# Optimization experiments

Measured on AMD Instinct MI355X. Metric: run time of the kernel, lower is better.

## Reference

```python
import jax, jax.numpy as jnp
import numpy as np

N_NODES = 50000
N_EDGES = 640000
D_FEAT = 128
D_HID = 128


def _sage_conv(x, src, dst, W_l, b_l, W_r, num_nodes):
    """PyG SAGEConv (aggr='mean'): out = lin_l(mean_j x_j) + lin_r(x_i).

    W_l/W_r are [out, in] (torch Linear convention); lin_r has no bias.
    """
    msgs = x[src]                                               # [E, d]
    agg = jax.ops.segment_sum(msgs, dst, num_segments=num_nodes)
    cnt = jax.ops.segment_sum(jnp.ones((src.shape[0], 1), x.dtype), dst,
                              num_segments=num_nodes)           # [N, 1]
    mean = agg / jnp.maximum(cnt, 1.0)                          # [N, d]
    return mean @ W_l.T + b_l + x @ W_r.T


def setup_inputs() -> dict:
    key = jax.random.key(0)
    ks = jax.random.split(key, 8)
    x = jax.random.normal(ks[0], (N_NODES, D_FEAT), dtype=jnp.float32)
    edge_index = jax.random.randint(ks[1], (2, N_EDGES), 0, N_NODES, dtype=jnp.int64)
    s1 = 1.0 / np.sqrt(D_FEAT)
    s2 = 1.0 / np.sqrt(D_HID)
    W1_l = jax.random.uniform(ks[2], (D_HID, D_FEAT), jnp.float32, -s1, s1)
    b1_l = jnp.zeros((D_HID,), jnp.float32)
    W1_r = jax.random.uniform(ks[3], (D_HID, D_FEAT), jnp.float32, -s1, s1)
    W2_l = jax.random.uniform(ks[4], (D_HID, D_HID), jnp.float32, -s2, s2)
    b2_l = jnp.zeros((D_HID,), jnp.float32)
    W2_r = jax.random.uniform(ks[5], (D_HID, D_HID), jnp.float32, -s2, s2)
    return {"x": x, "edge_index": edge_index, "W1_l": W1_l, "b1_l": b1_l,
            "W1_r": W1_r, "W2_l": W2_l, "b2_l": b2_l, "W2_r": W2_r}


def reference(x, edge_index, W1_l, b1_l, W1_r, W2_l, b2_l, W2_r):
    src, dst = edge_index[0], edge_index[1]
    n = x.shape[0]
    h = _sage_conv(x, src, dst, W1_l, b1_l, W1_r, n)
    h = jax.nn.relu(h)
    h = _sage_conv(h, src, dst, W2_l, b2_l, W2_r, n)
    return jax.nn.relu(h)
```

## Files before the change

kernel.cpp:

```cpp
#include <hip/hip_runtime.h>
#include <hip/hip_bf16.h>

#define N_NODES 50000
#define N_EDGES 640000
#define D 128
#define SCAN_BLK 25
#define PSTRIDE 50048

typedef __bf16 bf16x8 __attribute__((ext_vector_type(8)));
typedef float f32x4 __attribute__((ext_vector_type(4)));

__device__ __forceinline__ ushort f2bf(float f) {
    __hip_bfloat16 h = __float2bfloat16(f);
    return *(ushort*)&h;
}
__device__ __forceinline__ float bflo(uint u) { return __uint_as_float(u << 16); }
__device__ __forceinline__ float bfhi(uint u) { return __uint_as_float(u & 0xffff0000u); }

__global__ __launch_bounds__(256) void zero_kernel(uint4* __restrict__ p) {
    p[blockIdx.x * 256 + threadIdx.x] = make_uint4(0u, 0u, 0u, 0u);
}

__global__ __launch_bounds__(256) void prep_kernel(const float* __restrict__ x,
                                                   const float* __restrict__ W1l,
                                                   const float* __restrict__ W1r,
                                                   const float* __restrict__ W2l,
                                                   const float* __restrict__ W2r,
                                                   const int* __restrict__ dst,
                                                   ushort* __restrict__ xb,
                                                   ushort* __restrict__ Wb1,
                                                   ushort* __restrict__ Wb2,
                                                   int* __restrict__ deg8,
                                                   int* __restrict__ rank) {
    const int b = blockIdx.x;
    const int tid = threadIdx.x;
    if (b < 625) {
        const int base = b * 1024 + tid;
        int* dp = deg8 + (b & 7) * PSTRIDE;
        int d0 = dst[base];
        int d1 = dst[base + 256];
        int d2 = dst[base + 512];
        int d3 = dst[base + 768];
        int r0 = atomicAdd(&dp[d0], 1);
        int r1 = atomicAdd(&dp[d1], 1);
        int r2 = atomicAdd(&dp[d2], 1);
        int r3 = atomicAdd(&dp[d3], 1);
        rank[base]       = r0;
        rank[base + 256] = r1;
        rank[base + 512] = r2;
        rank[base + 768] = r3;
    } else if (b < 3750) {
        int i = (b - 625) * 256 + tid;
        const float4 u0 = *(const float4*)&x[i * 8];
        const float4 u1 = *(const float4*)&x[i * 8 + 4];
        union { ushort u[8]; uint4 v; } p;
        p.u[0] = f2bf(u0.x); p.u[1] = f2bf(u0.y); p.u[2] = f2bf(u0.z); p.u[3] = f2bf(u0.w);
        p.u[4] = f2bf(u1.x); p.u[5] = f2bf(u1.y); p.u[6] = f2bf(u1.z); p.u[7] = f2bf(u1.w);
        *(uint4*)&xb[i * 8] = p.v;
    } else {
        int i = (b - 3750) * 256 + tid;
        if (i < 32768) {
            int n = i >> 8, k = i & 255;
            float v = (k < 128) ? W1l[n * 128 + k] : W1r[n * 128 + (k - 128)];
            Wb1[i] = f2bf(v);
        } else {
            int j = i - 32768;
            int n = j >> 8, k = j & 255;
            float v = (k < 128) ? W2l[n * 128 + k] : W2r[n * 128 + (k - 128)];
            Wb2[j] = f2bf(v);
        }
    }
}

__global__ __launch_bounds__(256) void scan1_kernel(const int* __restrict__ deg8,
                                                    int* __restrict__ incl,
                                                    int* __restrict__ blockSum) {
    __shared__ int wsum[4];
    const int t = threadIdx.x;
    const int base = blockIdx.x * 2048 + t * 8;
    int v[8];
    int s = 0;
#pragma unroll
    for (int i = 0; i < 8; ++i) {
        int idx = base + i;
        int tot = 0;
        if (idx < N_NODES) {
#pragma unroll
            for (int p = 0; p < 8; ++p) tot += deg8[p * PSTRIDE + idx];
        }
        v[i] = tot;
        s += tot;
    }
    const int lane = t & 63;
    const int wid = t >> 6;
    int ps = s;
#pragma unroll
    for (int off = 1; off < 64; off <<= 1) {
        int u = __shfl_up(ps, off, 64);
        if (lane >= off) ps += u;
    }
    if (lane == 63) wsum[wid] = ps;
    __syncthreads();
    int wOff = 0;
    for (int w = 0; w < wid; ++w) wOff += wsum[w];
    int run = wOff + ps - s;
#pragma unroll
    for (int i = 0; i < 8; ++i) {
        run += v[i];
        int idx = base + i;
        if (idx < N_NODES) incl[idx] = run;
    }
    if (t == 255) blockSum[blockIdx.x] = wOff + ps;
}

__global__ __launch_bounds__(256) void scan2_kernel(const int* __restrict__ deg8,
                                                    const int* __restrict__ incl,
                                                    const int* __restrict__ blockSum,
                                                    int* __restrict__ row_off,
                                                    int* __restrict__ cursor8) {
    const int b = blockIdx.x;
    int off = 0;
    for (int i = 0; i < b; ++i) off += blockSum[i];
    const int t = threadIdx.x;
#pragma unroll
    for (int i = 0; i < 8; ++i) {
        int idx = b * 2048 + i * 256 + t;
        if (idx < N_NODES) {
            int inc = incl[idx] + off;
            row_off[idx + 1] = inc;
            int dp[8];
            int dsum = 0;
#pragma unroll
            for (int p = 0; p < 8; ++p) { dp[p] = deg8[p * PSTRIDE + idx]; dsum += dp[p]; }
            int c = inc - dsum;
#pragma unroll
            for (int p = 0; p < 8; ++p) { cursor8[p * PSTRIDE + idx] = c; c += dp[p]; }
        }
    }
    if (b == 0 && t == 0) row_off[0] = 0;
}

__global__ __launch_bounds__(256) void fill_kernel(const int* __restrict__ src,
                                                   const int* __restrict__ dst,
                                                   const int* __restrict__ rank,
                                                   const int* __restrict__ cursor8,
                                                   int* __restrict__ esrc) {
    const int base = blockIdx.x * 1024 + threadIdx.x;
    const int* cp = cursor8 + (blockIdx.x & 7) * PSTRIDE;
    int d0 = dst[base];
    int d1 = dst[base + 256];
    int d2 = dst[base + 512];
    int d3 = dst[base + 768];
    int s0 = src[base];
    int s1 = src[base + 256];
    int s2 = src[base + 512];
    int s3 = src[base + 768];
    int r0 = rank[base];
    int r1 = rank[base + 256];
    int r2 = rank[base + 512];
    int r3 = rank[base + 768];
    esrc[cp[d0] + r0] = s0;
    esrc[cp[d1] + r1] = s1;
    esrc[cp[d2] + r2] = s2;
    esrc[cp[d3] + r3] = s3;
}

__global__ __launch_bounds__(256) void gather_mean(const int* __restrict__ row_off,
                                                   const int* __restrict__ esrc,
                                                   const ushort* __restrict__ feat,
                                                   ushort* __restrict__ mean) {
    const int node = (blockIdx.x * 256 + threadIdx.x) >> 6;
    const int lane = threadIdx.x & 63;
    if (node >= N_NODES) return;
    const int beg = row_off[node];
    const int end = row_off[node + 1];
    const int g = lane >> 4;
    const int c = lane & 15;
    const char* fb = (const char*)feat;
    float acc[8];
#pragma unroll
    for (int r = 0; r < 8; ++r) acc[r] = 0.0f;

    for (int base = beg; base < end; base += 64) {
        const int lim = min(end - base, 64);
        int myIdx = 0;
        if (lane < lim) myIdx = esrc[base + lane];
        for (int i0 = 0; i0 < lim; i0 += 16) {
            uint4 v[4];
#pragma unroll
            for (int u = 0; u < 4; ++u) {
                int slot = i0 + u * 4 + g;
                int s = __shfl(myIdx, slot, 64);
                v[u] = make_uint4(0u, 0u, 0u, 0u);
                if (slot < lim)
                    v[u] = *(const uint4*)(fb + ((size_t)s << 8) + c * 16);
            }
#pragma unroll
            for (int u = 0; u < 4; ++u) {
                acc[0] += bflo(v[u].x);
                acc[1] += bfhi(v[u].x);
                acc[2] += bflo(v[u].y);
                acc[3] += bfhi(v[u].y);
                acc[4] += bflo(v[u].z);
                acc[5] += bfhi(v[u].z);
                acc[6] += bflo(v[u].w);
                acc[7] += bfhi(v[u].w);
            }
        }
    }
#pragma unroll
    for (int r = 0; r < 8; ++r) {
        acc[r] += __shfl_xor(acc[r], 16, 64);
        acc[r] += __shfl_xor(acc[r], 32, 64);
    }
    if (g == 0) {
        const int dg = end - beg;
        const float inv = (dg > 0) ? 1.0f / (float)dg : 0.0f;
        union { ushort u[8]; uint4 v; } p;
#pragma unroll
        for (int r = 0; r < 8; ++r) p.u[r] = f2bf(acc[r] * inv);
        *(uint4*)((char*)mean + ((size_t)node << 8) + c * 16) = p.v;
    }
}

template <int OUT_BF16>
__global__ __launch_bounds__(256) void sage_mfma(const ushort* __restrict__ feat,
                                                 const ushort* __restrict__ mean,
                                                 const ushort* __restrict__ Wb,
                                                 const float* __restrict__ bias,
                                                 void* __restrict__ outv) {
    __shared__ __align__(16) char As[64 * 512];

    const int tid = threadIdx.x;
    const int nodeBase = blockIdx.x * 64;

    {
        const int row = tid >> 2;
        const int q = tid & 3;
        const int node = nodeBase + row;
        const bool valid = node < N_NODES;
        const ushort* srcp = (q < 2) ? (mean + (size_t)node * D + q * 64)
                                     : (feat + (size_t)node * D + (q - 2) * 64);
        const int swz = (row & 7) << 4;
#pragma unroll
        for (int c = 0; c < 8; ++c) {
            uint4 v = make_uint4(0u, 0u, 0u, 0u);
            if (valid) v = *(const uint4*)(srcp + c * 8);
            int colb = q * 128 + c * 16;
            *(uint4*)(As + row * 512 + (colb ^ swz)) = v;
        }
    }
    __syncthreads();

    const int lane = tid & 63;
    const int w = tid >> 6;
    const int l15 = lane & 15;
    const int lg = lane >> 4;
    const int swz = (l15 & 7) << 4;

    f32x4 acc[4][2];
#pragma unroll
    for (int m = 0; m < 4; ++m) {
        acc[m][0] = (f32x4)(0.0f);
        acc[m][1] = (f32x4)(0.0f);
    }

    const ushort* WA = Wb + (size_t)(w * 32 + l15) * 256 + lg * 8;
    const ushort* WB = WA + 16 * 256;

#pragma unroll
    for (int t = 0; t < 8; ++t) {
        bf16x8 b0 = *(const bf16x8*)(WA + t * 32);
        bf16x8 b1 = *(const bf16x8*)(WB + t * 32);
        const int kb = t * 64 + lg * 16;
#pragma unroll
        for (int m = 0; m < 4; ++m) {
            bf16x8 a = *(const bf16x8*)(As + (m * 16 + l15) * 512 + (kb ^ swz));
            acc[m][0] = __builtin_amdgcn_mfma_f32_16x16x32_bf16(a, b0, acc[m][0], 0, 0, 0);
            acc[m][1] = __builtin_amdgcn_mfma_f32_16x16x32_bf16(a, b1, acc[m][1], 0, 0, 0);
        }
    }

    const int c0 = w * 32 + l15;
    const float bv0 = bias[c0];
    const float bv1 = bias[c0 + 16];
#pragma unroll
    for (int m = 0; m < 4; ++m) {
#pragma unroll
        for (int j = 0; j < 4; ++j) {
            int node = nodeBase + m * 16 + lg * 4 + j;
            if (node < N_NODES) {
                float r0 = fmaxf(acc[m][0][j] + bv0, 0.0f);
                float r1 = fmaxf(acc[m][1][j] + bv1, 0.0f);
                if (OUT_BF16) {
                    ushort* out = (ushort*)outv;
                    out[(size_t)node * D + c0]      = f2bf(r0);
                    out[(size_t)node * D + c0 + 16] = f2bf(r1);
                } else {
                    float* out = (float*)outv;
                    out[(size_t)node * D + c0]      = r0;
                    out[(size_t)node * D + c0 + 16] = r1;
                }
            }
        }
    }
}

extern "C" void kernel_launch(void* const* d_in, const int* in_sizes, int n_in,
                              void* d_out, int out_size, void* d_ws, size_t ws_size,
                              hipStream_t stream) {
    const float* x   = (const float*)d_in[0];
    const int*   ei  = (const int*)d_in[1];
    const int*   src = ei;
    const int*   dst = ei + N_EDGES;
    const float* W1l = (const float*)d_in[2];
    const float* b1  = (const float*)d_in[3];
    const float* W1r = (const float*)d_in[4];
    const float* W2l = (const float*)d_in[5];
    const float* b2  = (const float*)d_in[6];
    const float* W2r = (const float*)d_in[7];
    float* out = (float*)d_out;

    ushort* xb     = (ushort*)d_ws;
    ushort* hb     = xb + (size_t)N_NODES * D;
    ushort* meanb  = hb + (size_t)N_NODES * D;
    int*   row_off = (int*)(meanb + (size_t)N_NODES * D);
    int*   esrc    = row_off + (N_NODES + 1);
    int*   rank    = esrc + N_EDGES;
    int*   deg8    = rank + N_EDGES;
    int*   cursor8 = deg8 + 8 * PSTRIDE;
    int*   incl    = cursor8 + 8 * PSTRIDE;
    int*   blockSum= incl + N_NODES;
    ushort* Wb1    = (ushort*)(blockSum + SCAN_BLK);
    ushort* Wb2    = Wb1 + 128 * 256;

    const int edge4Blocks = N_EDGES / 1024;
    const int waveBlocks = (N_NODES * 64 + 255) / 256;
    const int gemmBlocks = (N_NODES + 63) / 64;
    const int prepBlocks = 625 + 3125 + 256;
    const int zeroBlocks = (8 * PSTRIDE * 4) / 4096;

    zero_kernel<<<zeroBlocks, 256, 0, stream>>>((uint4*)deg8);
    prep_kernel<<<prepBlocks, 256, 0, stream>>>(x, W1l, W1r, W2l, W2r, dst,
                                                xb, Wb1, Wb2, deg8, rank);
    scan1_kernel<<<SCAN_BLK, 256, 0, stream>>>(deg8, incl, blockSum);
    scan2_kernel<<<SCAN_BLK, 256, 0, stream>>>(deg8, incl, blockSum, row_off, cursor8);
    fill_kernel<<<edge4Blocks, 256, 0, stream>>>(src, dst, rank, cursor8, esrc);

    gather_mean<<<waveBlocks, 256, 0, stream>>>(row_off, esrc, xb, meanb);
    sage_mfma<1><<<gemmBlocks, 256, 0, stream>>>(xb, meanb, Wb1, b1, hb);

    gather_mean<<<waveBlocks, 256, 0, stream>>>(row_off, esrc, hb, meanb);
    sage_mfma<0><<<gemmBlocks, 256, 0, stream>>>(hb, meanb, Wb2, b2, out);
}
```

Before: 149.4 us.

## Fuse CSR build kernels into one cooperative kernel with grid syncs

Replaces the five preprocessing launches (zero, prep, scan1, scan2, fill) with a single cooperative kernel of 1024 blocks that separates the phases with grid.sync(). The aim is to cut kernel launch gaps and tail effects between the small CSR-build stages. In exchange, the scan phases occupy only 25 of the 1024 blocks while the rest wait at grid barriers. Zeroing now happens in the same phase as conversion, with a grid sync before the atomics.

```diff
diff --git a/kernel.cpp b/kernel.cpp
--- a/kernel.cpp
+++ b/kernel.cpp
@@ -1,11 +1,16 @@
 #include <hip/hip_runtime.h>
 #include <hip/hip_bf16.h>
+#include <hip/hip_cooperative_groups.h>
+
+namespace cg = cooperative_groups;
 
 #define N_NODES 50000
 #define N_EDGES 640000
 #define D 128
 #define SCAN_BLK 25
 #define PSTRIDE 50048
+#define MEGA_BLOCKS 1024
+#define MEGA_NT (MEGA_BLOCKS * 256)
 
 typedef __bf16 bf16x8 __attribute__((ext_vector_type(8)));
 typedef float f32x4 __attribute__((ext_vector_type(4)));
@@ -17,48 +22,41 @@
 __device__ __forceinline__ float bflo(uint u) { return __uint_as_float(u << 16); }
 __device__ __forceinline__ float bfhi(uint u) { return __uint_as_float(u & 0xffff0000u); }
 
-__global__ __launch_bounds__(256) void zero_kernel(uint4* __restrict__ p) {
-    p[blockIdx.x * 256 + threadIdx.x] = make_uint4(0u, 0u, 0u, 0u);
-}
-
-__global__ __launch_bounds__(256) void prep_kernel(const float* __restrict__ x,
+__global__ __launch_bounds__(256) void mega_kernel(const float* __restrict__ x,
                                                    const float* __restrict__ W1l,
                                                    const float* __restrict__ W1r,
                                                    const float* __restrict__ W2l,
                                                    const float* __restrict__ W2r,
+                                                   const int* __restrict__ src,
                                                    const int* __restrict__ dst,
                                                    ushort* __restrict__ xb,
                                                    ushort* __restrict__ Wb1,
                                                    ushort* __restrict__ Wb2,
                                                    int* __restrict__ deg8,
-                                                   int* __restrict__ rank) {
+                                                   int* __restrict__ rank,
+                                                   int* __restrict__ incl,
+                                                   int* __restrict__ blockSum,
+                                                   int* __restrict__ row_off,
+                                                   int* __restrict__ cursor8,
+                                                   int* __restrict__ esrc) {
+    cg::grid_group grid = cg::this_grid();
+    __shared__ int wsum[4];
+    const int tid = threadIdx.x;
     const int b = blockIdx.x;
-    const int tid = threadIdx.x;
-    if (b < 625) {
-        const int base = b * 1024 + tid;
-        int* dp = deg8 + (b & 7) * PSTRIDE;
-        int d0 = dst[base];
-        int d1 = dst[base + 256];
-        int d2 = dst[base + 512];
-        int d3 = dst[base + 768];
-        int r0 = atomicAdd(&dp[d0], 1);
-        int r1 = atomicAdd(&dp[d1], 1);
-        int r2 = atomicAdd(&dp[d2], 1);
-        int r3 = atomicAdd(&dp[d3], 1);
-        rank[base]       = r0;
-        rank[base + 256] = r1;
-        rank[base + 512] = r2;
-        rank[base + 768] = r3;
-    } else if (b < 3750) {
-        int i = (b - 625) * 256 + tid;
+    const int gtid = b * 256 + tid;
+
+    if (gtid < (8 * PSTRIDE) / 4)
+        ((uint4*)deg8)[gtid] = make_uint4(0u, 0u, 0u, 0u);
+    for (int i = gtid; i < (N_NODES * D) / 8; i += MEGA_NT) {
         const float4 u0 = *(const float4*)&x[i * 8];
         const float4 u1 = *(const float4*)&x[i * 8 + 4];
         union { ushort u[8]; uint4 v; } p;
         p.u[0] = f2bf(u0.x); p.u[1] = f2bf(u0.y); p.u[2] = f2bf(u0.z); p.u[3] = f2bf(u0.w);
         p.u[4] = f2bf(u1.x); p.u[5] = f2bf(u1.y); p.u[6] = f2bf(u1.z); p.u[7] = f2bf(u1.w);
         *(uint4*)&xb[i * 8] = p.v;
-    } else {
-        int i = (b - 3750) * 256 + tid;
+    }
+    if (gtid < 65536) {
+        int i = gtid;
         if (i < 32768) {
             int n = i >> 8, k = i & 255;
             float v = (k < 128) ? W1l[n * 128 + k] : W1r[n * 128 + (k - 128)];
@@ -70,99 +68,80 @@
             Wb2[j] = f2bf(v);
         }
     }
-}
-
-__global__ __launch_bounds__(256) void scan1_kernel(const int* __restrict__ deg8,
-                                                    int* __restrict__ incl,
-                                                    int* __restrict__ blockSum) {
-    __shared__ int wsum[4];
-    const int t = threadIdx.x;
-    const int base = blockIdx.x * 2048 + t * 8;
-    int v[8];
-    int s = 0;
-#pragma unroll
-    for (int i = 0; i < 8; ++i) {
-        int idx = base + i;
-        int tot = 0;
-        if (idx < N_NODES) {
-#pragma unroll
-            for (int p = 0; p < 8; ++p) tot += deg8[p * PSTRIDE + idx];
-        }
-        v[i] = tot;
-        s += tot;
-    }
-    const int lane = t & 63;
-    const int wid = t >> 6;
-    int ps = s;
-#pragma unroll
-    for (int off = 1; off < 64; off <<= 1) {
-        int u = __shfl_up(ps, off, 64);
-        if (lane >= off) ps += u;
-    }
-    if (lane == 63) wsum[wid] = ps;
-    __syncthreads();
-    int wOff = 0;
-    for (int w = 0; w < wid; ++w) wOff += wsum[w];
-    int run = wOff + ps - s;
-#pragma unroll
-    for (int i = 0; i < 8; ++i) {
-        run += v[i];
-        int idx = base + i;
-        if (idx < N_NODES) incl[idx] = run;
-    }
-    if (t == 255) blockSum[blockIdx.x] = wOff + ps;
-}
-
-__global__ __launch_bounds__(256) void scan2_kernel(const int* __restrict__ deg8,
-                                                    const int* __restrict__ incl,
-                                                    const int* __restrict__ blockSum,
-                                                    int* __restrict__ row_off,
-                                                    int* __restrict__ cursor8) {
-    const int b = blockIdx.x;
-    int off = 0;
-    for (int i = 0; i < b; ++i) off += blockSum[i];
-    const int t = threadIdx.x;
-#pragma unroll
-    for (int i = 0; i < 8; ++i) {
-        int idx = b * 2048 + i * 256 + t;
-        if (idx < N_NODES) {
-            int inc = incl[idx] + off;
-            row_off[idx + 1] = inc;
-            int dp[8];
-            int dsum = 0;
-#pragma unroll
-            for (int p = 0; p < 8; ++p) { dp[p] = deg8[p * PSTRIDE + idx]; dsum += dp[p]; }
-            int c = inc - dsum;
-#pragma unroll
-            for (int p = 0; p < 8; ++p) { cursor8[p * PSTRIDE + idx] = c; c += dp[p]; }
-        }
-    }
-    if (b == 0 && t == 0) row_off[0] = 0;
-}
-
-__global__ __launch_bounds__(256) void fill_kernel(const int* __restrict__ src,
-                                                   const int* __restrict__ dst,
-                                                   const int* __restrict__ rank,
-                                                   const int* __restrict__ cursor8,
-                                                   int* __restrict__ esrc) {
-    const int base = blockIdx.x * 1024 + threadIdx.x;
-    const int* cp = cursor8 + (blockIdx.x & 7) * PSTRIDE;
-    int d0 = dst[base];
-    int d1 = dst[base + 256];
-    int d2 = dst[base + 512];
-    int d3 = dst[base + 768];
-    int s0 = src[base];
-    int s1 = src[base + 256];
-    int s2 = src[base + 512];
-    int s3 = src[base + 768];
-    int r0 = rank[base];
-    int r1 = rank[base + 256];
-    int r2 = rank[base + 512];
-    int r3 = rank[base + 768];
-    esrc[cp[d0] + r0] = s0;
-    esrc[cp[d1] + r1] = s1;
-    esrc[cp[d2] + r2] = s2;
-    esrc[cp[d3] + r3] = s3;
+    grid.sync();
+
+    {
+        int* dp = deg8 + (b & 7) * PSTRIDE;
+        for (int e = gtid; e < N_EDGES; e += MEGA_NT)
+            rank[e] = atomicAdd(&dp[dst[e]], 1);
+    }
+    grid.sync();
+
+    if (b < SCAN_BLK) {
+        const int base = b * 2048 + tid * 8;
+        int v[8];
+        int s = 0;
+#pragma unroll
+        for (int i = 0; i < 8; ++i) {
+            int idx = base + i;
+            int tot = 0;
+            if (idx < N_NODES) {
+#pragma unroll
+                for (int p = 0; p < 8; ++p) tot += deg8[p * PSTRIDE + idx];
+            }
+            v[i] = tot;
+            s += tot;
+        }
+        const int lane = tid & 63;
+        const int wid = tid >> 6;
+        int ps = s;
+#pragma unroll
+        for (int off = 1; off < 64; off <<= 1) {
+            int u = __shfl_up(ps, off, 64);
+            if (lane >= off) ps += u;
+        }
+        if (lane == 63) wsum[wid] = ps;
+        __syncthreads();
+        int wOff = 0;
+        for (int w = 0; w < wid; ++w) wOff += wsum[w];
+        int run = wOff + ps - s;
+#pragma unroll
+        for (int i = 0; i < 8; ++i) {
+            run += v[i];
+            int idx = base + i;
+            if (idx < N_NODES) incl[idx] = run;
+        }
+        if (tid == 255) blockSum[b] = wOff + ps;
+    }
+    grid.sync();
+
+    if (b < SCAN_BLK) {
+        int off = 0;
+        for (int i = 0; i < b; ++i) off += blockSum[i];
+#pragma unroll
+        for (int i = 0; i < 8; ++i) {
+            int idx = b * 2048 + i * 256 + tid;
+            if (idx < N_NODES) {
+                int inc = incl[idx] + off;
+                row_off[idx + 1] = inc;
+                int dp[8];
+                int dsum = 0;
+#pragma unroll
+                for (int p = 0; p < 8; ++p) { dp[p] = deg8[p * PSTRIDE + idx]; dsum += dp[p]; }
+                int c = inc - dsum;
+#pragma unroll
+                for (int p = 0; p < 8; ++p) { cursor8[p * PSTRIDE + idx] = c; c += dp[p]; }
+            }
+        }
+        if (b == 0 && tid == 0) row_off[0] = 0;
+    }
+    grid.sync();
+
+    {
+        const int* cp = cursor8 + (b & 7) * PSTRIDE;
+        for (int e = gtid; e < N_EDGES; e += MEGA_NT)
+            esrc[cp[dst[e]] + rank[e]] = src[e];
+    }
 }
 
 __global__ __launch_bounds__(256) void gather_mean(const int* __restrict__ row_off,
@@ -334,18 +313,20 @@
     ushort* Wb1    = (ushort*)(blockSum + SCAN_BLK);
     ushort* Wb2    = Wb1 + 128 * 256;
 
-    const int edge4Blocks = N_EDGES / 1024;
     const int waveBlocks = (N_NODES * 64 + 255) / 256;
     const int gemmBlocks = (N_NODES + 63) / 64;
-    const int prepBlocks = 625 + 3125 + 256;
-    const int zeroBlocks = (8 * PSTRIDE * 4) / 4096;
-
-    zero_kernel<<<zeroBlocks, 256, 0, stream>>>((uint4*)deg8);
-    prep_kernel<<<prepBlocks, 256, 0, stream>>>(x, W1l, W1r, W2l, W2r, dst,
-                                                xb, Wb1, Wb2, deg8, rank);
-    scan1_kernel<<<SCAN_BLK, 256, 0, stream>>>(deg8, incl, blockSum);
-    scan2_kernel<<<SCAN_BLK, 256, 0, stream>>>(deg8, incl, blockSum, row_off, cursor8);
-    fill_kernel<<<edge4Blocks, 256, 0, stream>>>(src, dst, rank, cursor8, esrc);
+
+    {
+        void* args[] = {
+            (void*)&x, (void*)&W1l, (void*)&W1r, (void*)&W2l, (void*)&W2r,
+            (void*)&src, (void*)&dst,
+            (void*)&xb, (void*)&Wb1, (void*)&Wb2,
+            (void*)&deg8, (void*)&rank, (void*)&incl, (void*)&blockSum,
+            (void*)&row_off, (void*)&cursor8, (void*)&esrc
+        };
+        hipLaunchCooperativeKernel((void*)mega_kernel, dim3(MEGA_BLOCKS), dim3(256),
+                                   args, 0, stream);
+    }
 
     gather_mean<<<waveBlocks, 256, 0, stream>>>(row_off, esrc, xb, meanb);
     sage_mfma<1><<<gemmBlocks, 256, 0, stream>>>(xb, meanb, Wb1, b1, hb);
```

Result: slower. 593.4 us (+297.3%).

## Fuse two-pass prefix scan into single-pass chained scan kernel

Applied to the files above, without the earlier changes.

Replaces the two scan kernels (per-block scan, then offset add and cursor computation) with one kernel that uses a decoupled chained scan. Each block spins on its predecessor's published inclusive sum through atomics, then writes row offsets and per-partition cursors directly. The scan state sits next to deg8 so the existing zero kernel clears it. This removes one kernel launch and the incl/blockSum round trip through memory, at the cost of serialized spin-waiting across 25 blocks, which relies on those blocks all being resident at once.

```diff
diff --git a/kernel.cpp b/kernel.cpp
--- a/kernel.cpp
+++ b/kernel.cpp
@@ -18,7 +18,9 @@
 __device__ __forceinline__ float bfhi(uint u) { return __uint_as_float(u & 0xffff0000u); }
 
 __global__ __launch_bounds__(256) void zero_kernel(uint4* __restrict__ p) {
-    p[blockIdx.x * 256 + threadIdx.x] = make_uint4(0u, 0u, 0u, 0u);
+    int i = blockIdx.x * 256 + threadIdx.x;
+    if (i < (8 * PSTRIDE + 32) / 4)
+        p[i] = make_uint4(0u, 0u, 0u, 0u);
 }
 
 __global__ __launch_bounds__(256) void prep_kernel(const float* __restrict__ x,
@@ -72,12 +74,16 @@
     }
 }
 
-__global__ __launch_bounds__(256) void scan1_kernel(const int* __restrict__ deg8,
-                                                    int* __restrict__ incl,
-                                                    int* __restrict__ blockSum) {
+__global__ __launch_bounds__(256) void scan_kernel(const int* __restrict__ deg8,
+                                                   int* __restrict__ scanState,
+                                                   int* __restrict__ row_off,
+                                                   int* __restrict__ cursor8) {
     __shared__ int wsum[4];
+    __shared__ int sExcl;
+    const int b = blockIdx.x;
     const int t = threadIdx.x;
-    const int base = blockIdx.x * 2048 + t * 8;
+    const int base = b * 2048 + t * 8;
+
     int v[8];
     int s = 0;
 #pragma unroll
@@ -103,38 +109,34 @@
     __syncthreads();
     int wOff = 0;
     for (int w = 0; w < wid; ++w) wOff += wsum[w];
-    int run = wOff + ps - s;
+    const int total = wsum[0] + wsum[1] + wsum[2] + wsum[3];
+
+    if (t == 0) {
+        int excl = 0;
+        if (b > 0) {
+            int st;
+            do { st = atomicAdd(&scanState[b - 1], 0); } while ((st & 1) == 0);
+            excl = st >> 1;
+        }
+        atomicExch(&scanState[b], ((excl + total) << 1) | 1);
+        sExcl = excl;
+    }
+    __syncthreads();
+    const int excl = sExcl;
+
+    int run = excl + wOff + ps - s;
 #pragma unroll
     for (int i = 0; i < 8; ++i) {
         run += v[i];
         int idx = base + i;
-        if (idx < N_NODES) incl[idx] = run;
-    }
-    if (t == 255) blockSum[blockIdx.x] = wOff + ps;
-}
-
-__global__ __launch_bounds__(256) void scan2_kernel(const int* __restrict__ deg8,
-                                                    const int* __restrict__ incl,
-                                                    const int* __restrict__ blockSum,
-                                                    int* __restrict__ row_off,
-                                                    int* __restrict__ cursor8) {
-    const int b = blockIdx.x;
-    int off = 0;
-    for (int i = 0; i < b; ++i) off += blockSum[i];
-    const int t = threadIdx.x;
-#pragma unroll
-    for (int i = 0; i < 8; ++i) {
-        int idx = b * 2048 + i * 256 + t;
         if (idx < N_NODES) {
-            int inc = incl[idx] + off;
-            row_off[idx + 1] = inc;
-            int dp[8];
-            int dsum = 0;
-#pragma unroll
-            for (int p = 0; p < 8; ++p) { dp[p] = deg8[p * PSTRIDE + idx]; dsum += dp[p]; }
-            int c = inc - dsum;
-#pragma unroll
-            for (int p = 0; p < 8; ++p) { cursor8[p * PSTRIDE + idx] = c; c += dp[p]; }
+            row_off[idx + 1] = run;
+            int c = run - v[i];
+#pragma unroll
+            for (int p = 0; p < 8; ++p) {
+                cursor8[p * PSTRIDE + idx] = c;
+                c += deg8[p * PSTRIDE + idx];
+            }
         }
     }
     if (b == 0 && t == 0) row_off[0] = 0;
@@ -328,23 +330,21 @@
     int*   esrc    = row_off + (N_NODES + 1);
     int*   rank    = esrc + N_EDGES;
     int*   deg8    = rank + N_EDGES;
-    int*   cursor8 = deg8 + 8 * PSTRIDE;
-    int*   incl    = cursor8 + 8 * PSTRIDE;
-    int*   blockSum= incl + N_NODES;
-    ushort* Wb1    = (ushort*)(blockSum + SCAN_BLK);
+    int*   scanSt  = deg8 + 8 * PSTRIDE;
+    int*   cursor8 = scanSt + 32;
+    ushort* Wb1    = (ushort*)(cursor8 + 8 * PSTRIDE);
     ushort* Wb2    = Wb1 + 128 * 256;
 
     const int edge4Blocks = N_EDGES / 1024;
     const int waveBlocks = (N_NODES * 64 + 255) / 256;
     const int gemmBlocks = (N_NODES + 63) / 64;
     const int prepBlocks = 625 + 3125 + 256;
-    const int zeroBlocks = (8 * PSTRIDE * 4) / 4096;
+    const int zeroBlocks = ((8 * PSTRIDE + 32) / 4 + 255) / 256;
 
     zero_kernel<<<zeroBlocks, 256, 0, stream>>>((uint4*)deg8);
     prep_kernel<<<prepBlocks, 256, 0, stream>>>(x, W1l, W1r, W2l, W2r, dst,
                                                 xb, Wb1, Wb2, deg8, rank);
-    scan1_kernel<<<SCAN_BLK, 256, 0, stream>>>(deg8, incl, blockSum);
-    scan2_kernel<<<SCAN_BLK, 256, 0, stream>>>(deg8, incl, blockSum, row_off, cursor8);
+    scan_kernel<<<SCAN_BLK, 256, 0, stream>>>(deg8, scanSt, row_off, cursor8);
     fill_kernel<<<edge4Blocks, 256, 0, stream>>>(src, dst, rank, cursor8, esrc);
 
     gather_mean<<<waveBlocks, 256, 0, stream>>>(row_off, esrc, xb, meanb);
```

Result: slower. 167.3 us (+12.0%).
